# Performance work log

Hardware: AMD Instinct MI355X
Metric: run time of the kernel (lower is better)

## Reference

```python
import jax, jax.numpy as jnp
import numpy as np
jax.config.update("jax_enable_x64", True)

IN_FEATURES = 4096
OUT_FEATURES = 4096
BATCH, SEQ = 4, 2048


def _gen_weight(seed, out_features, in_features):
    # Stand-in for the Rust FastGMemContext PRNG fill: deterministic fp64
    # weight regenerated from the 64-bit seed on every call (never stored).
    k = jax.random.key(seed)
    return jax.random.normal(k, (out_features, in_features), dtype=jnp.float64)


def setup_inputs() -> dict:
    key = jax.random.key(0)
    kx, _ = jax.random.split(key)
    x = jax.random.normal(kx, (BATCH, SEQ, IN_FEATURES), dtype=jnp.float32)
    bias = jnp.zeros((OUT_FEATURES,), dtype=jnp.float32)
    return {"x": x, "bias": bias, "seed": 42}


def reference(x, bias, seed):
    out_features = bias.shape[0]
    in_features = x.shape[-1]
    w = _gen_weight(seed, out_features, in_features)  # [out, in] fp64
    # fp64 matmul, downcast to input dtype, then add bias (as in GMemLinear)
    out = jnp.matmul(x.astype(jnp.float64), w.T).astype(x.dtype)
    return out + bias
```

## Files before the change

kernel.cpp:

```cpp
#include <hip/hip_runtime.h>
#include <hip/hip_bf16.h>
#include <cstdint>
#include <math.h>


typedef __bf16  bf16x8 __attribute__((ext_vector_type(8)));
typedef float   f32x4  __attribute__((ext_vector_type(4)));
typedef unsigned short u16x8 __attribute__((ext_vector_type(8)));

__device__ __forceinline__ unsigned short f2bf_rne(float f) {
  uint32_t x = __float_as_uint(f);
  uint32_t r = (x + 0x7FFFu + ((x >> 16) & 1u)) >> 16;
  return (unsigned short)r;
}

__device__ __forceinline__ void threefry2x32(uint32_t k0, uint32_t k1,
                                             uint32_t x0, uint32_t x1,
                                             uint32_t& o0, uint32_t& o1) {
  uint32_t ks0 = k0, ks1 = k1, ks2 = k0 ^ k1 ^ 0x1BD11BDAu;
  uint32_t ks[3] = {ks0, ks1, ks2};
  x0 += ks0; x1 += ks1;
  const uint32_t rot0[4] = {13u, 15u, 26u, 6u};
  const uint32_t rot1[4] = {17u, 29u, 16u, 24u};
#pragma unroll
  for (int i = 0; i < 5; ++i) {
    const uint32_t* r = (i & 1) ? rot1 : rot0;
#pragma unroll
    for (int j = 0; j < 4; ++j) {
      x0 += x1;
      x1 = (x1 << r[j]) | (x1 >> (32u - r[j]));
      x1 ^= x0;
    }
    x0 += ks[(i + 1) % 3];
    x1 += ks[(i + 2) % 3] + (uint32_t)(i + 1);
  }
  o0 = x0; o1 = x1;
}

__device__ __forceinline__ float normal_from_bits_f32(uint64_t m52) {
  const bool pos = (m52 >> 51) & 1;
  uint64_t dmin = pos ? ((1ull << 52) - m52) : m52;
  uint32_t hi = (uint32_t)(dmin >> 27);
  uint32_t lo = (uint32_t)(dmin & 0x7FFFFFFu);
  float oma = fmaf((float)hi, 0x1p-24f, (float)lo * 0x1p-51f);
  oma = fmaxf(oma, 0x1p-53f);
  float au  = 1.0f - oma;
  float u   = pos ? au : -au;
  float opa = 2.0f - oma;
  float t   = oma * opa;
  float wf  = -__logf(t);
  float x;
  if (wf < 15.5f) {
    float w, p;
    if (wf < 5.0f) {
      w = wf - 2.5f;
      p = 2.81022636e-08f;
      p = 3.43273939e-07f + p * w;
      p = -3.5233877e-06f + p * w;
      p = -4.39150654e-06f + p * w;
      p = 0.00021858087f + p * w;
      p = -0.00125372503f + p * w;
      p = -0.00417768164f + p * w;
      p = 0.246640727f + p * w;
      p = 1.50140941f + p * w;
    } else {
      w = sqrtf(wf) - 3.0f;
      p = -0.000200214257f;
      p = 0.000100950558f + p * w;
      p = 0.00134934322f + p * w;
      p = -0.00367342844f + p * w;
      p = 0.00573950773f + p * w;
      p = -0.0076224613f + p * w;
      p = 0.00943887047f + p * w;
      p = 1.00167406f + p * w;
      p = 2.83297682f + p * w;
    }
    x = p * u;
  } else {
    float L = wf + __logf(opa);
    float r = sqrtf(L);
    r = sqrtf(L - __logf(r) - 0.57236494f);
    r = sqrtf(L - __logf(r) - 0.57236494f);
    x = pos ? r : -r;
  }
  return 1.41421356f * x;
}

__device__ __forceinline__ void cast_phase(const float* __restrict__ X,
                                           unsigned short* __restrict__ Y,
                                           int nx, int gid, int gsz) {
  const int n8 = nx >> 3;
  for (int q = gid; q < n8; q += gsz) {
    const float4* p = (const float4*)(X + ((size_t)q << 3));
    float4 a = p[0], b = p[1];
    u16x8 o;
    o[0] = f2bf_rne(a.x); o[1] = f2bf_rne(a.y);
    o[2] = f2bf_rne(a.z); o[3] = f2bf_rne(a.w);
    o[4] = f2bf_rne(b.x); o[5] = f2bf_rne(b.y);
    o[6] = f2bf_rne(b.z); o[7] = f2bf_rne(b.w);
    *(u16x8*)(Y + ((size_t)q << 3)) = o;
  }
}

__device__ __forceinline__ void gen_phase(unsigned short* __restrict__ W,
                                          uint32_t k1, int nw, int gid, int gsz) {
  const uint32_t k0 = 0u;
  const int nq = nw >> 2;
  for (int q = gid; q < nq; q += gsz) {
    ushort4 outv;
    unsigned short tmp[4];
#pragma unroll
    for (int j = 0; j < 4; ++j) {
      uint32_t e = ((uint32_t)q << 2) + (uint32_t)j;
      uint32_t o0, o1;
      threefry2x32(k0, k1, 0u, e, o0, o1);
      uint64_t bits = ((uint64_t)o0 << 32) | (uint64_t)o1;
      tmp[j] = f2bf_rne(normal_from_bits_f32(bits >> 12));
    }
    outv.x = tmp[0]; outv.y = tmp[1]; outv.z = tmp[2]; outv.w = tmp[3];
    *(ushort4*)(W + ((size_t)q << 2)) = outv;
  }
}

__global__ void gen_and_cast(const float* __restrict__ X,
                             unsigned short* __restrict__ Y,
                             unsigned short* __restrict__ W,
                             const int* __restrict__ seedp,
                             int nx, int nw) {
  const int gsz = (int)(gridDim.x * blockDim.x);
  const int gid = (int)(blockIdx.x * blockDim.x + threadIdx.x);
  const uint32_t k1 = (uint32_t)seedp[0];
  if (blockIdx.x & 1) {
    cast_phase(X, Y, nx, gid, gsz);
    gen_phase(W, k1, nw, gid, gsz);
  } else {
    gen_phase(W, k1, nw, gid, gsz);
    cast_phase(X, Y, nx, gid, gsz);
  }
}


__device__ __forceinline__ void gload_lds16(const void* g, void* l) {
  __builtin_amdgcn_global_load_lds(
      (const __attribute__((address_space(1))) unsigned int*)g,
      (__attribute__((address_space(3))) unsigned int*)l, 16, 0, 0);
}

__device__ __forceinline__ uint32_t lds_u32(void* p) {
  return (uint32_t)(uintptr_t)(__attribute__((address_space(3))) char*)p;
}

template <int OFF>
__device__ __forceinline__ bf16x8 dsr16(uint32_t a) {
  bf16x8 r;
  asm volatile("ds_read_b128 %0, %1 offset:%2" : "=v"(r) : "v"(a), "i"(OFF));
  return r;
}

__global__ __launch_bounds__(512, 2) void gemm256(
    const unsigned short* __restrict__ A,
    const unsigned short* __restrict__ B,
    const float* __restrict__ bias,
    float* __restrict__ C,
    int M, int N, int K) {
  __shared__ __align__(1024) char lds[131072];

  const int nwg = (int)gridDim.x;
  int wg = (int)blockIdx.x;
  wg = (wg & 7) * (nwg >> 3) + (wg >> 3);
  const int ntn = N >> 8;
  const int tm = wg / ntn, tn = wg - tm * ntn;

  const int tid = (int)threadIdx.x;
  const int w = tid >> 6, l = tid & 63;
  const int wr = w >> 2, wc = w & 3;
  const int l15 = l & 15;

  int laneRd = (l15 << 6) | ((l >> 4) << 4);
  laneRd ^= ((l15 >> 1) & 3) << 4;
  const int stRow = l >> 2;
  const int stCol = (((l & 3) ^ ((l >> 3) & 3)) << 4);

  const char* Ag = (const char*)A;
  const char* Bg = (const char*)B;
  const long rowA0 = (long)tm * 256;
  const long rowB0 = (long)tn * 256;
  const long Kb = (long)K;

  const uint32_t lds0  = lds_u32(&lds[0]);
  const uint32_t aBase = lds0 + (uint32_t)(wr * 8192 + laneRd);
  const uint32_t bBase = lds0 + 16384u + (uint32_t)(wc * 4096 + laneRd);

#define STAGE_A(kt_, cs_)                                                     \
  _Pragma("unroll")                                                           \
  for (int i_ = 0; i_ < 2; ++i_) {                                            \
    const int u_ = w * 2 + i_;                                                \
    gload_lds16(Ag + 2 * ((rowA0 + u_ * 16 + stRow) * Kb + (long)(kt_) * 32) + stCol, \
                &lds[(cs_) * 32768 + u_ * 1024]);                             \
  }
#define STAGE_B(kt_, cs_)                                                     \
  _Pragma("unroll")                                                           \
  for (int i_ = 0; i_ < 2; ++i_) {                                            \
    const int u_ = w * 2 + i_;                                                \
    gload_lds16(Bg + 2 * ((rowB0 + u_ * 16 + stRow) * Kb + (long)(kt_) * 32) + stCol, \
                &lds[(cs_) * 32768 + 16384 + u_ * 1024]);                     \
  }

#define PF_A03(cn_)                                                           \
  {                                                                           \
    const uint32_t aB = aBase + (cn_) * 32768u;                               \
    aq[0] = dsr16<0>(aB);    aq[1] = dsr16<1024>(aB);                         \
    aq[2] = dsr16<2048>(aB); aq[3] = dsr16<3072>(aB);                         \
  }
#define PF_REST(cn_)                                                          \
  {                                                                           \
    const uint32_t aB = aBase + (cn_) * 32768u;                               \
    const uint32_t bB = bBase + (cn_) * 32768u;                               \
    bq[0] = dsr16<0>(bB);    bq[1] = dsr16<1024>(bB);                         \
    bq[2] = dsr16<2048>(bB); bq[3] = dsr16<3072>(bB);                         \
    aq[4] = dsr16<4096>(aB); aq[5] = dsr16<5120>(aB);                         \
    aq[6] = dsr16<6144>(aB); aq[7] = dsr16<7168>(aB);                         \
  }

#define MFMA16(base_)                                                         \
  _Pragma("unroll")                                                           \
  for (int mi = 0; mi < 4; ++mi)                                              \
    _Pragma("unroll")                                                         \
    for (int ni = 0; ni < 4; ++ni)                                            \
      acc[(base_) + mi][ni] = __builtin_amdgcn_mfma_f32_16x16x32_bf16(        \
          aq[(base_) + mi], bq[ni], acc[(base_) + mi][ni], 0, 0, 0);

#define TILE_BODY(c_, kt_, vm_, st_, pf_)                                     \
  {                                                                           \
    asm volatile("s_waitcnt lgkmcnt(4)" ::: "memory");                        \
    __builtin_amdgcn_sched_barrier(0);                                        \
    __builtin_amdgcn_s_setprio(1);                                            \
    MFMA16(0)                                                                 \
    __builtin_amdgcn_s_setprio(0);                                            \
    if (pf_) { PF_A03(((c_) + 1) & 3) }                                       \
    if (st_) { STAGE_A((kt_) + 3, ((c_) + 3) & 3) }                           \
    if (pf_) { asm volatile("s_waitcnt lgkmcnt(4)" ::: "memory"); }           \
    else     { asm volatile("s_waitcnt lgkmcnt(0)" ::: "memory"); }           \
    __builtin_amdgcn_sched_barrier(0);                                        \
    __builtin_amdgcn_s_setprio(1);                                            \
    MFMA16(4)                                                                 \
    __builtin_amdgcn_s_setprio(0);                                            \
    if (pf_) { PF_REST(((c_) + 1) & 3) }                                      \
    if (st_) { STAGE_B((kt_) + 3, ((c_) + 3) & 3) }                           \
    asm volatile("s_waitcnt vmcnt(" #vm_ ")" ::: "memory");                   \
    __builtin_amdgcn_sched_barrier(0);                                        \
    __builtin_amdgcn_s_barrier();                                             \
  }

  f32x4 acc[8][4];
#pragma unroll
  for (int i = 0; i < 8; ++i)
#pragma unroll
    for (int j = 0; j < 4; ++j) acc[i][j] = (f32x4){0.f, 0.f, 0.f, 0.f};

  bf16x8 aq[8], bq[4];

  const int NTt = K >> 5;

  STAGE_A(0, 0) STAGE_B(0, 0)
  STAGE_A(1, 1) STAGE_B(1, 1)
  STAGE_A(2, 2) STAGE_B(2, 2)
  asm volatile("s_waitcnt vmcnt(4)" ::: "memory");
  __builtin_amdgcn_sched_barrier(0);
  __builtin_amdgcn_s_barrier();
  PF_A03(0)
  PF_REST(0)

  int kt = 0;
  for (; kt + 7 < NTt; kt += 4) {
    TILE_BODY(0, kt,     4, 1, 1)
    TILE_BODY(1, kt + 1, 4, 1, 1)
    TILE_BODY(2, kt + 2, 4, 1, 1)
    TILE_BODY(3, kt + 3, 4, 1, 1)
  }
  TILE_BODY(0, kt,     4, 1, 1)
  TILE_BODY(1, kt + 1, 0, 0, 1)
  TILE_BODY(2, kt + 2, 0, 0, 1)
  TILE_BODY(3, kt + 3, 0, 0, 0)

#pragma unroll
  for (int ni = 0; ni < 4; ++ni) {
    const int col = tn * 256 + wc * 64 + ni * 16 + l15;
    const float bv = bias[col];
#pragma unroll
    for (int mi = 0; mi < 8; ++mi) {
      const int r0 = tm * 256 + wr * 128 + mi * 16 + ((l >> 4) << 2);
      f32x4 v = acc[mi][ni];
#pragma unroll
      for (int j = 0; j < 4; ++j)
        C[(size_t)(r0 + j) * N + col] = v[j] + bv;
    }
  }
#undef STAGE_A
#undef STAGE_B
#undef PF_A03
#undef PF_REST
#undef MFMA16
#undef TILE_BODY
}

extern "C" void kernel_launch(void* const* d_in, const int* in_sizes, int n_in,
                              void* d_out, int out_size, void* d_ws, size_t ws_size,
                              hipStream_t stream) {
  const float* x    = (const float*)d_in[0];
  const float* bias = (const float*)d_in[1];
  const int*   seed = (const int*)d_in[2];
  float* out = (float*)d_out;

  const int K = 4096;
  const int N = in_sizes[1];
  const int M = in_sizes[0] / K;

  unsigned short* W  = (unsigned short*)d_ws;
  unsigned short* Xb = W + (size_t)N * K;

  gen_and_cast<<<2048, 256, 0, stream>>>(x, Xb, W, seed, M * K, N * K);

  dim3 grid((M / 256) * (N / 256));
  gemm256<<<grid, 512, 0, stream>>>((const unsigned short*)Xb,
                                    (const unsigned short*)W,
                                    bias, out, M, N, K);
}
```

Before: 300.5 us.

## Restructure GEMM main loop into K=64 double-buffered tiles with 8-phase interleaving

Replaces the 4-stage K=32 LDS ring with two K=64 buffers and splits each tile into four phases that read LDS fragments, issue a slice of the next global-to-LDS loads, barrier, then run MFMAs. The intent is a finer-grained interleave of global loads, LDS reads and MFMA work, with fewer barriers per K element. It adds a barrier per phase, waits on lgkmcnt(0) before every MFMA group, and doubles the LDS footprint per buffer, which may lower occupancy or serialize LDS latency.

```diff
diff --git a/kernel.cpp b/kernel.cpp
--- a/kernel.cpp
+++ b/kernel.cpp
@@ -187,68 +187,72 @@
   const long rowB0 = (long)tn * 256;
   const long Kb = (long)K;
 
-  const uint32_t lds0  = lds_u32(&lds[0]);
-  const uint32_t aBase = lds0 + (uint32_t)(wr * 8192 + laneRd);
-  const uint32_t bBase = lds0 + 16384u + (uint32_t)(wc * 4096 + laneRd);
-
-#define STAGE_A(kt_, cs_)                                                     \
+  const uint32_t lds0 = lds_u32(&lds[0]);
+  const uint32_t bA0r = lds0 + (uint32_t)(wr * 16384 + laneRd);
+  const uint32_t bB0r = lds0 + 32768u + (uint32_t)(wc * 8192 + laneRd);
+  const uint32_t bA1r = bA0r + 65536u;
+  const uint32_t bB1r = bB0r + 65536u;
+
+#define STAGE_AH(kt_, h_, boff_)                                              \
+  {                                                                           \
+    const int rb_ = (h_) * 8 + w;                                             \
+    _Pragma("unroll")                                                         \
+    for (int i_ = 0; i_ < 2; ++i_)                                            \
+      gload_lds16(Ag + 2 * ((rowA0 + rb_ * 16 + stRow) * Kb +                 \
+                            (long)(kt_) * 64 + i_ * 32) + stCol,              \
+                  &lds[(boff_) + (rb_ * 2 + i_) * 1024]);                     \
+  }
+#define STAGE_BH(kt_, h_, boff_)                                              \
+  {                                                                           \
+    const int cb_ = (h_) * 8 + w;                                             \
+    _Pragma("unroll")                                                         \
+    for (int i_ = 0; i_ < 2; ++i_)                                            \
+      gload_lds16(Bg + 2 * ((rowB0 + cb_ * 16 + stRow) * Kb +                 \
+                            (long)(kt_) * 64 + i_ * 32) + stCol,              \
+                  &lds[(boff_) + (cb_ * 2 + i_) * 1024]);                     \
+  }
+
+#define RD_B(bB_)                                                             \
+  bq[0][0] = dsr16<0>(bB_);    bq[0][1] = dsr16<1024>(bB_);                   \
+  bq[1][0] = dsr16<2048>(bB_); bq[1][1] = dsr16<3072>(bB_);                   \
+  bq[2][0] = dsr16<4096>(bB_); bq[2][1] = dsr16<5120>(bB_);                   \
+  bq[3][0] = dsr16<6144>(bB_); bq[3][1] = dsr16<7168>(bB_);
+
+#define RD_A(q_, bA_)                                                         \
+  aq[0][0] = dsr16<((q_) * 4 + 0) * 1024>(bA_);                               \
+  aq[0][1] = dsr16<((q_) * 4 + 1) * 1024>(bA_);                               \
+  aq[1][0] = dsr16<((q_) * 4 + 2) * 1024>(bA_);                               \
+  aq[1][1] = dsr16<((q_) * 4 + 3) * 1024>(bA_);
+
+#define MFMAQ(q_)                                                             \
   _Pragma("unroll")                                                           \
-  for (int i_ = 0; i_ < 2; ++i_) {                                            \
-    const int u_ = w * 2 + i_;                                                \
-    gload_lds16(Ag + 2 * ((rowA0 + u_ * 16 + stRow) * Kb + (long)(kt_) * 32) + stCol, \
-                &lds[(cs_) * 32768 + u_ * 1024]);                             \
-  }
-#define STAGE_B(kt_, cs_)                                                     \
-  _Pragma("unroll")                                                           \
-  for (int i_ = 0; i_ < 2; ++i_) {                                            \
-    const int u_ = w * 2 + i_;                                                \
-    gload_lds16(Bg + 2 * ((rowB0 + u_ * 16 + stRow) * Kb + (long)(kt_) * 32) + stCol, \
-                &lds[(cs_) * 32768 + 16384 + u_ * 1024]);                     \
-  }
-
-#define PF_A03(cn_)                                                           \
+  for (int kh = 0; kh < 2; ++kh)                                              \
+    _Pragma("unroll")                                                         \
+    for (int i = 0; i < 2; ++i)                                               \
+      _Pragma("unroll")                                                       \
+      for (int ni = 0; ni < 4; ++ni)                                          \
+        acc[2 * (q_) + i][ni] = __builtin_amdgcn_mfma_f32_16x16x32_bf16(      \
+            aq[i][kh], bq[ni][kh], acc[2 * (q_) + i][ni], 0, 0, 0);
+
+#define VM4 asm volatile("s_waitcnt vmcnt(4)" ::: "memory");                  \
+  __builtin_amdgcn_sched_barrier(0);
+#define VM0 asm volatile("s_waitcnt vmcnt(0)" ::: "memory");                  \
+  __builtin_amdgcn_sched_barrier(0);
+#define NOVM
+
+#define PH(q_, bA_, bB_, STG, VMW)                                            \
   {                                                                           \
-    const uint32_t aB = aBase + (cn_) * 32768u;                               \
-    aq[0] = dsr16<0>(aB);    aq[1] = dsr16<1024>(aB);                         \
-    aq[2] = dsr16<2048>(aB); aq[3] = dsr16<3072>(aB);                         \
-  }
-#define PF_REST(cn_)                                                          \
-  {                                                                           \
-    const uint32_t aB = aBase + (cn_) * 32768u;                               \
-    const uint32_t bB = bBase + (cn_) * 32768u;                               \
-    bq[0] = dsr16<0>(bB);    bq[1] = dsr16<1024>(bB);                         \
-    bq[2] = dsr16<2048>(bB); bq[3] = dsr16<3072>(bB);                         \
-    aq[4] = dsr16<4096>(aB); aq[5] = dsr16<5120>(aB);                         \
-    aq[6] = dsr16<6144>(aB); aq[7] = dsr16<7168>(aB);                         \
-  }
-
-#define MFMA16(base_)                                                         \
-  _Pragma("unroll")                                                           \
-  for (int mi = 0; mi < 4; ++mi)                                              \
-    _Pragma("unroll")                                                         \
-    for (int ni = 0; ni < 4; ++ni)                                            \
-      acc[(base_) + mi][ni] = __builtin_amdgcn_mfma_f32_16x16x32_bf16(        \
-          aq[(base_) + mi], bq[ni], acc[(base_) + mi][ni], 0, 0, 0);
-
-#define TILE_BODY(c_, kt_, vm_, st_, pf_)                                     \
-  {                                                                           \
-    asm volatile("s_waitcnt lgkmcnt(4)" ::: "memory");                        \
+    bf16x8 aq[2][2];                                                          \
+    if ((q_) == 0) { RD_B(bB_) }                                              \
+    RD_A(q_, bA_)                                                             \
+    STG                                                                       \
+    VMW                                                                       \
+    __builtin_amdgcn_s_barrier();                                             \
+    asm volatile("s_waitcnt lgkmcnt(0)" ::: "memory");                        \
     __builtin_amdgcn_sched_barrier(0);                                        \
     __builtin_amdgcn_s_setprio(1);                                            \
-    MFMA16(0)                                                                 \
+    MFMAQ(q_)                                                                 \
     __builtin_amdgcn_s_setprio(0);                                            \
-    if (pf_) { PF_A03(((c_) + 1) & 3) }                                       \
-    if (st_) { STAGE_A((kt_) + 3, ((c_) + 3) & 3) }                           \
-    if (pf_) { asm volatile("s_waitcnt lgkmcnt(4)" ::: "memory"); }           \
-    else     { asm volatile("s_waitcnt lgkmcnt(0)" ::: "memory"); }           \
-    __builtin_amdgcn_sched_barrier(0);                                        \
-    __builtin_amdgcn_s_setprio(1);                                            \
-    MFMA16(4)                                                                 \
-    __builtin_amdgcn_s_setprio(0);                                            \
-    if (pf_) { PF_REST(((c_) + 1) & 3) }                                      \
-    if (st_) { STAGE_B((kt_) + 3, ((c_) + 3) & 3) }                           \
-    asm volatile("s_waitcnt vmcnt(" #vm_ ")" ::: "memory");                   \
-    __builtin_amdgcn_sched_barrier(0);                                        \
     __builtin_amdgcn_s_barrier();                                             \
   }
 
@@ -258,30 +262,34 @@
 #pragma unroll
     for (int j = 0; j < 4; ++j) acc[i][j] = (f32x4){0.f, 0.f, 0.f, 0.f};
 
-  bf16x8 aq[8], bq[4];
-
-  const int NTt = K >> 5;
-
-  STAGE_A(0, 0) STAGE_B(0, 0)
-  STAGE_A(1, 1) STAGE_B(1, 1)
-  STAGE_A(2, 2) STAGE_B(2, 2)
-  asm volatile("s_waitcnt vmcnt(4)" ::: "memory");
-  __builtin_amdgcn_sched_barrier(0);
+  bf16x8 bq[4][2];
+
+  const int NTt = K >> 6;
+
+  STAGE_AH(0, 0, 0)      STAGE_AH(0, 1, 0)
+  STAGE_BH(0, 0, 32768)  STAGE_BH(0, 1, 32768)
+  STAGE_BH(1, 0, 98304)  STAGE_BH(1, 1, 98304)
+  VM4
   __builtin_amdgcn_s_barrier();
-  PF_A03(0)
-  PF_REST(0)
-
-  int kt = 0;
-  for (; kt + 7 < NTt; kt += 4) {
-    TILE_BODY(0, kt,     4, 1, 1)
-    TILE_BODY(1, kt + 1, 4, 1, 1)
-    TILE_BODY(2, kt + 2, 4, 1, 1)
-    TILE_BODY(3, kt + 3, 4, 1, 1)
-  }
-  TILE_BODY(0, kt,     4, 1, 1)
-  TILE_BODY(1, kt + 1, 0, 0, 1)
-  TILE_BODY(2, kt + 2, 0, 0, 1)
-  TILE_BODY(3, kt + 3, 0, 0, 0)
+
+  for (int kt = 0; kt < NTt - 2; kt += 2) {
+    PH(0, bA0r, bB0r, STAGE_AH(kt + 1, 0, 65536), NOVM)
+    PH(1, bA0r, bB0r, STAGE_AH(kt + 1, 1, 65536), NOVM)
+    PH(2, bA0r, bB0r, STAGE_BH(kt + 2, 0, 32768), NOVM)
+    PH(3, bA0r, bB0r, STAGE_BH(kt + 2, 1, 32768), VM4)
+    PH(0, bA1r, bB1r, STAGE_AH(kt + 2, 0, 0), NOVM)
+    PH(1, bA1r, bB1r, STAGE_AH(kt + 2, 1, 0), NOVM)
+    PH(2, bA1r, bB1r, STAGE_BH(kt + 3, 0, 98304), NOVM)
+    PH(3, bA1r, bB1r, STAGE_BH(kt + 3, 1, 98304), VM4)
+  }
+  PH(0, bA0r, bB0r, STAGE_AH(NTt - 1, 0, 65536), NOVM)
+  PH(1, bA0r, bB0r, STAGE_AH(NTt - 1, 1, 65536), NOVM)
+  PH(2, bA0r, bB0r, NOVM, NOVM)
+  PH(3, bA0r, bB0r, NOVM, VM0)
+  PH(0, bA1r, bB1r, NOVM, NOVM)
+  PH(1, bA1r, bB1r, NOVM, NOVM)
+  PH(2, bA1r, bB1r, NOVM, NOVM)
+  PH(3, bA1r, bB1r, NOVM, NOVM)
 
 #pragma unroll
   for (int ni = 0; ni < 4; ++ni) {
@@ -296,12 +304,15 @@
         C[(size_t)(r0 + j) * N + col] = v[j] + bv;
     }
   }
-#undef STAGE_A
-#undef STAGE_B
-#undef PF_A03
-#undef PF_REST
-#undef MFMA16
-#undef TILE_BODY
+#undef STAGE_AH
+#undef STAGE_BH
+#undef RD_A
+#undef RD_B
+#undef MFMAQ
+#undef VM4
+#undef VM0
+#undef NOVM
+#undef PH
 }
 
 extern "C" void kernel_launch(void* const* d_in, const int* in_sizes, int n_in,
```

After: 297.4 us. About the same (-1.1%).

## Switch GEMM inner loop from 16x16x32 to 32x32x16 bf16 MFMA

Applied to the files above, without the earlier changes.

Replaces the 16x16x32 bf16 MFMA tiling with 32x32x16 MFMAs. The LDS read addressing, register fragments, accumulator layout and epilogue store mapping are all reorganised to match. Each K-tile now splits into two 16-wide k-halves instead of two row groups. The aim is fewer MFMA issues and fewer LDS reads per FLOP, in exchange for a different swizzled read pattern that may cause bank conflicts and a more scattered output store layout.

```diff
diff --git a/kernel.cpp b/kernel.cpp
--- a/kernel.cpp
+++ b/kernel.cpp
@@ -4,8 +4,8 @@
 #include <math.h>
 
 
-typedef __bf16  bf16x8 __attribute__((ext_vector_type(8)));
-typedef float   f32x4  __attribute__((ext_vector_type(4)));
+typedef __bf16  bf16x8  __attribute__((ext_vector_type(8)));
+typedef float   f32x16  __attribute__((ext_vector_type(16)));
 typedef unsigned short u16x8 __attribute__((ext_vector_type(8)));
 
 __device__ __forceinline__ unsigned short f2bf_rne(float f) {
@@ -174,10 +174,11 @@
   const int tid = (int)threadIdx.x;
   const int w = tid >> 6, l = tid & 63;
   const int wr = w >> 2, wc = w & 3;
-  const int l15 = l & 15;
-
-  int laneRd = (l15 << 6) | ((l >> 4) << 4);
-  laneRd ^= ((l15 >> 1) & 3) << 4;
+  const int l15   = l & 15;
+  const int lhalf = (l >> 4) & 1;
+  const int lhi   = l >> 5;
+  const int xsw   = (l15 >> 1) & 3;
+
   const int stRow = l >> 2;
   const int stCol = (((l & 3) ^ ((l >> 3) & 3)) << 4);
 
@@ -187,9 +188,13 @@
   const long rowB0 = (long)tn * 256;
   const long Kb = (long)K;
 
-  const uint32_t lds0  = lds_u32(&lds[0]);
-  const uint32_t aBase = lds0 + (uint32_t)(wr * 8192 + laneRd);
-  const uint32_t bBase = lds0 + 16384u + (uint32_t)(wc * 4096 + laneRd);
+  const uint32_t lds0 = lds_u32(&lds[0]);
+  const uint32_t koff0 = (uint32_t)(((0 * 2 + lhi) ^ xsw) << 4);
+  const uint32_t koff1 = (uint32_t)(((1 * 2 + lhi) ^ xsw) << 4);
+  const uint32_t aRd = lds0 + (uint32_t)(wr * 8192 + lhalf * 1024 + l15 * 64);
+  const uint32_t bRd = lds0 + 16384u + (uint32_t)(wc * 4096 + lhalf * 1024 + l15 * 64);
+  const uint32_t aB0 = aRd + koff0, aB1 = aRd + koff1;
+  const uint32_t bB0 = bRd + koff0, bB1 = bRd + koff1;
 
 #define STAGE_A(kt_, cs_)                                                     \
   _Pragma("unroll")                                                           \
@@ -206,59 +211,62 @@
                 &lds[(cs_) * 32768 + 16384 + u_ * 1024]);                     \
   }
 
-#define PF_A03(cn_)                                                           \
+#define PF_C0(cn_)                                                            \
   {                                                                           \
-    const uint32_t aB = aBase + (cn_) * 32768u;                               \
-    aq[0] = dsr16<0>(aB);    aq[1] = dsr16<1024>(aB);                         \
-    aq[2] = dsr16<2048>(aB); aq[3] = dsr16<3072>(aB);                         \
-  }
-#define PF_REST(cn_)                                                          \
+    const uint32_t aB_ = aB0 + (cn_) * 32768u;                                \
+    const uint32_t bB_ = bB0 + (cn_) * 32768u;                                \
+    aq[0][0] = dsr16<0>(aB_);    aq[0][1] = dsr16<2048>(aB_);                 \
+    aq[0][2] = dsr16<4096>(aB_); aq[0][3] = dsr16<6144>(aB_);                 \
+    bq[0][0] = dsr16<0>(bB_);    bq[0][1] = dsr16<2048>(bB_);                 \
+  }
+#define PF_C1(cn_)                                                            \
   {                                                                           \
-    const uint32_t aB = aBase + (cn_) * 32768u;                               \
-    const uint32_t bB = bBase + (cn_) * 32768u;                               \
-    bq[0] = dsr16<0>(bB);    bq[1] = dsr16<1024>(bB);                         \
-    bq[2] = dsr16<2048>(bB); bq[3] = dsr16<3072>(bB);                         \
-    aq[4] = dsr16<4096>(aB); aq[5] = dsr16<5120>(aB);                         \
-    aq[6] = dsr16<6144>(aB); aq[7] = dsr16<7168>(aB);                         \
-  }
-
-#define MFMA16(base_)                                                         \
+    const uint32_t aB_ = aB1 + (cn_) * 32768u;                                \
+    const uint32_t bB_ = bB1 + (cn_) * 32768u;                                \
+    aq[1][0] = dsr16<0>(aB_);    aq[1][1] = dsr16<2048>(aB_);                 \
+    aq[1][2] = dsr16<4096>(aB_); aq[1][3] = dsr16<6144>(aB_);                 \
+    bq[1][0] = dsr16<0>(bB_);    bq[1][1] = dsr16<2048>(bB_);                 \
+  }
+
+#define MFMAQ(ks_)                                                            \
   _Pragma("unroll")                                                           \
   for (int mi = 0; mi < 4; ++mi)                                              \
     _Pragma("unroll")                                                         \
-    for (int ni = 0; ni < 4; ++ni)                                            \
-      acc[(base_) + mi][ni] = __builtin_amdgcn_mfma_f32_16x16x32_bf16(        \
-          aq[(base_) + mi], bq[ni], acc[(base_) + mi][ni], 0, 0, 0);
+    for (int nj = 0; nj < 2; ++nj)                                            \
+      acc[mi][nj] = __builtin_amdgcn_mfma_f32_32x32x16_bf16(                  \
+          aq[ks_][mi], bq[ks_][nj], acc[mi][nj], 0, 0, 0);
 
 #define TILE_BODY(c_, kt_, vm_, st_, pf_)                                     \
   {                                                                           \
-    asm volatile("s_waitcnt lgkmcnt(4)" ::: "memory");                        \
+    asm volatile("s_waitcnt lgkmcnt(6)" ::: "memory");                        \
     __builtin_amdgcn_sched_barrier(0);                                        \
     __builtin_amdgcn_s_setprio(1);                                            \
-    MFMA16(0)                                                                 \
+    MFMAQ(0)                                                                  \
     __builtin_amdgcn_s_setprio(0);                                            \
-    if (pf_) { PF_A03(((c_) + 1) & 3) }                                       \
+    if (pf_) { PF_C0(((c_) + 1) & 3) }                                        \
     if (st_) { STAGE_A((kt_) + 3, ((c_) + 3) & 3) }                           \
-    if (pf_) { asm volatile("s_waitcnt lgkmcnt(4)" ::: "memory"); }           \
+    if (pf_) { asm volatile("s_waitcnt lgkmcnt(6)" ::: "memory"); }           \
     else     { asm volatile("s_waitcnt lgkmcnt(0)" ::: "memory"); }           \
     __builtin_amdgcn_sched_barrier(0);                                        \
     __builtin_amdgcn_s_setprio(1);                                            \
-    MFMA16(4)                                                                 \
+    MFMAQ(1)                                                                  \
     __builtin_amdgcn_s_setprio(0);                                            \
-    if (pf_) { PF_REST(((c_) + 1) & 3) }                                      \
+    if (pf_) { PF_C1(((c_) + 1) & 3) }                                        \
     if (st_) { STAGE_B((kt_) + 3, ((c_) + 3) & 3) }                           \
     asm volatile("s_waitcnt vmcnt(" #vm_ ")" ::: "memory");                   \
     __builtin_amdgcn_sched_barrier(0);                                        \
     __builtin_amdgcn_s_barrier();                                             \
   }
 
-  f32x4 acc[8][4];
-#pragma unroll
-  for (int i = 0; i < 8; ++i)
-#pragma unroll
-    for (int j = 0; j < 4; ++j) acc[i][j] = (f32x4){0.f, 0.f, 0.f, 0.f};
-
-  bf16x8 aq[8], bq[4];
+  f32x16 acc[4][2];
+#pragma unroll
+  for (int i = 0; i < 4; ++i)
+#pragma unroll
+    for (int j = 0; j < 2; ++j)
+#pragma unroll
+      for (int e = 0; e < 16; ++e) acc[i][j][e] = 0.f;
+
+  bf16x8 aq[2][4], bq[2][2];
 
   const int NTt = K >> 5;
 
@@ -268,8 +276,8 @@
   asm volatile("s_waitcnt vmcnt(4)" ::: "memory");
   __builtin_amdgcn_sched_barrier(0);
   __builtin_amdgcn_s_barrier();
-  PF_A03(0)
-  PF_REST(0)
+  PF_C0(0)
+  PF_C1(0)
 
   int kt = 0;
   for (; kt + 7 < NTt; kt += 4) {
@@ -284,23 +292,25 @@
   TILE_BODY(3, kt + 3, 0, 0, 0)
 
 #pragma unroll
-  for (int ni = 0; ni < 4; ++ni) {
-    const int col = tn * 256 + wc * 64 + ni * 16 + l15;
+  for (int nj = 0; nj < 2; ++nj) {
+    const int col = tn * 256 + wc * 64 + nj * 32 + (l & 31);
     const float bv = bias[col];
 #pragma unroll
-    for (int mi = 0; mi < 8; ++mi) {
-      const int r0 = tm * 256 + wr * 128 + mi * 16 + ((l >> 4) << 2);
-      f32x4 v = acc[mi][ni];
-#pragma unroll
-      for (int j = 0; j < 4; ++j)
-        C[(size_t)(r0 + j) * N + col] = v[j] + bv;
+    for (int mi = 0; mi < 4; ++mi) {
+      const int r0 = tm * 256 + wr * 128 + mi * 32 + (lhi << 2);
+      f32x16 v = acc[mi][nj];
+#pragma unroll
+      for (int reg = 0; reg < 16; ++reg) {
+        const int row = r0 + (reg & 3) + 8 * (reg >> 2);
+        C[(size_t)row * N + col] = v[reg] + bv;
+      }
     }
   }
 #undef STAGE_A
 #undef STAGE_B
-#undef PF_A03
-#undef PF_REST
-#undef MFMA16
+#undef PF_C0
+#undef PF_C1
+#undef MFMAQ
 #undef TILE_BODY
 }
 
```

Measured after the change: 316.3 us. +5.3%, slower.
